# Performance work log

Hardware: AMD Instinct MI355X
Metric: run time of the kernel (lower is better)

The kernel has to match this reference:

```python
import jax, jax.numpy as jnp
import numpy as np


def setup_inputs() -> dict:
    key = jax.random.key(0)
    k1, k2 = jax.random.split(key)
    bg = jax.random.normal(k1, (1, 4, 32, 32, 32, 16), dtype=jnp.float32)
    gm = jax.random.uniform(k2, (1, 1, 128, 128, 128), dtype=jnp.float32)
    return {"bg": bg, "gm": gm}


def _prep(coord, size):
    # replicate boundary: clamp sample coords into [0, size-1]
    coord = jnp.clip(coord, 0.0, float(size - 1))
    i0f = jnp.floor(coord)
    frac = coord - i0f
    i0 = i0f.astype(jnp.int32)
    i1 = jnp.minimum(i0 + 1, size - 1)
    return i0, i1, frac


def reference(bg, gm):
    # bg: (n,c,h,w,d,up) 4D bilateral grid; gm: (n,1,gh,gw,gd) guidance volume
    n, c, h, w, d, up = bg.shape
    _, _, gh, gw, gd = gm.shape
    f32 = jnp.float32

    # voxel-space sample coordinates (module: hg/(h_img-1) * (h-1) etc.)
    x = jnp.arange(gh, dtype=f32) * (f32(h - 1) / f32(gh - 1))  # (gh,)
    y = jnp.arange(gw, dtype=f32) * (f32(w - 1) / f32(gw - 1))  # (gw,)
    z = jnp.arange(gd, dtype=f32) * (f32(d - 1) / f32(gd - 1))  # (gd,)
    t = gm[:, 0] * f32(up - 1)                                   # (n,gh,gw,gd)

    x0, x1, fx = _prep(x, h)
    y0, y1, fy = _prep(y, w)
    z0, z1, fz = _prep(z, d)
    t0, t1, ft = _prep(t, up)

    def opts(i0, i1, frac, shape):
        i0 = i0.reshape(shape); i1 = i1.reshape(shape); frac = frac.reshape(shape)
        return [(i0, 1.0 - frac), (i1, frac)]

    xo = opts(x0, x1, fx, (1, gh, 1, 1))
    yo = opts(y0, y1, fy, (1, 1, gw, 1))
    zo = opts(z0, z1, fz, (1, 1, 1, gd))
    to = [(t0, 1.0 - ft), (t1, ft)]  # already (n,gh,gw,gd)

    bidx = jnp.arange(n)[:, None, None, None]        # (n,1,1,1)
    bgc = jnp.moveaxis(bg, 1, -1)                    # (n,h,w,d,up,c)

    acc = jnp.zeros((n, gh, gw, gd, c), dtype=bg.dtype)
    # 2^4 = 16 corners of quadri-linear interpolation (grid_pull order=1)
    for ix, wx in xo:
        for iy, wy in yo:
            for iz, wz in zo:
                for it, wt in to:
                    vals = bgc[bidx, ix, iy, iz, it]         # (n,gh,gw,gd,c)
                    wgt = (wx * wy * wz * wt)[..., None]     # (n,gh,gw,gd,1)
                    acc = acc + vals * wgt
    return jnp.moveaxis(acc, -1, 1)                  # (n,c,gh,gw,gd)
```

## Files before the change

### kernel.cpp

```cpp
#include <hip/hip_runtime.h>
#include <hip/hip_fp16.h>


#define S_ (31.0f / 127.0f)
#define CH_STRIDE 524288
#define TOTAL 2097152

#define NX 4
#define NY 4
#define NZ 6
#define NNODES (NX * NY * NZ)
#define NODE_DW 68
#define LDS_DW (NNODES * NODE_DW)

__global__ __launch_bounds__(256, 5) void bgrid_slice_v4(
    const float* __restrict__ bg,
    const float* __restrict__ gm,
    float* __restrict__ out)
{
    __shared__ __align__(16) float lds[LDS_DW];

    const int tid = threadIdx.x;
    const int b = blockIdx.x;
    const int bk = b & 7;
    const int bj = (b >> 3) & 15;
    const int bi = b >> 7;

    const int i0 = bi * 8, j0 = bj * 8, k0 = bk * 16;
    const int x_base = (int)((float)i0 * S_);
    const int y_base = (int)((float)j0 * S_);
    const int z_base = (int)((float)k0 * S_);

    for (int q = tid; q < NNODES * 16; q += 256) {
        const int node = q >> 4;
        const int s = q & 15;
        const int a = node / (NY * NZ);
        const int rem = node - a * (NY * NZ);
        const int bb = rem / NZ;
        const int cz = rem - bb * NZ;
        const int gx = min(x_base + a, 31);
        const int gy = min(y_base + bb, 31);
        const int gz = min(z_base + cz, 31);
        const int gbase = (((gx * 32 + gy) * 32 + gz) << 4) + s;

        const float c0 = bg[gbase];
        const float c1 = bg[gbase + CH_STRIDE];
        const float c2 = bg[gbase + 2 * CH_STRIDE];
        const float c3 = bg[gbase + 3 * CH_STRIDE];

        float2 pk;
        pk.x = __builtin_bit_cast(float, __floats2half2_rn(c0, c1));
        pk.y = __builtin_bit_cast(float, __floats2half2_rn(c2, c3));

        const int nb = node * NODE_DW;
        *(float2*)&lds[nb + (s << 2)] = pk;
        if (s > 0)  *(float2*)&lds[nb + ((s - 1) << 2) + 2] = pk;
        if (s == 15) *(float2*)&lds[nb + (15 << 2) + 2] = pk;
    }
    __syncthreads();

    const int kq = tid & 3;
    const int lj = (tid >> 2) & 7;
    const int li = tid >> 5;
    const int i = i0 + li, j = j0 + lj;
    const int kk = k0 + (kq << 2);

    const float xf = fminf((float)i * S_, 31.0f);
    const float yf = fminf((float)j * S_, 31.0f);
    const int x0g = (int)xf; const float fx = xf - (float)x0g;
    const int y0g = (int)yf; const float fy = yf - (float)y0g;
    const int xi0 = x0g - x_base, xi1 = min(x0g + 1, 31) - x_base;
    const int yi0 = y0g - y_base, yi1 = min(y0g + 1, 31) - y_base;

    const int AX0 = xi0 * (NY * NZ * NODE_DW);
    const int AX1 = xi1 * (NY * NZ * NODE_DW);
    const int BY0 = yi0 * (NZ * NODE_DW);
    const int BY1 = yi1 * (NZ * NODE_DW);

    const float wx1 = fx, wx0 = 1.0f - fx;
    const float wy1 = fy, wy0 = 1.0f - fy;
    const __half2 W00 = __float2half2_rn(wx0 * wy0);
    const __half2 W01 = __float2half2_rn(wx0 * wy1);
    const __half2 W10 = __float2half2_rn(wx1 * wy0);
    const __half2 W11 = __float2half2_rn(wx1 * wy1);

    const int idx = (i << 14) | (j << 7) | kk;
    const float4 g4 = *(const float4*)&gm[idx];

    float o0[4], o1[4], o2[4], o3[4];

#pragma unroll
    for (int v = 0; v < 4; ++v) {
        const float g = (v == 0) ? g4.x : (v == 1) ? g4.y : (v == 2) ? g4.z : g4.w;
        float t = fminf(fmaxf(g * 15.0f, 0.0f), 15.0f);
        const int t0 = min((int)t, 14);
        const float ft = t - (float)t0;
        const __half2 ft2 = __float2half2_rn(ft);

        const float zf = fminf((float)(kk + v) * S_, 31.0f);
        const int z0g = (int)zf;
        const float fz = zf - (float)z0g;
        const int zi0 = z0g - z_base;
        const int zi1 = min(z0g + 1, 31) - z_base;
        const __half2 fz2 = __float2half2_rn(fz);

        const int CZ0 = zi0 * NODE_DW + (t0 << 2);
        const int CZ1 = zi1 * NODE_DW + (t0 << 2);

        const float4 a00 = *(const float4*)&lds[AX0 + BY0 + CZ0];
        const float4 a01 = *(const float4*)&lds[AX0 + BY1 + CZ0];
        const float4 a10 = *(const float4*)&lds[AX1 + BY0 + CZ0];
        const float4 a11 = *(const float4*)&lds[AX1 + BY1 + CZ0];
        const float4 b00 = *(const float4*)&lds[AX0 + BY0 + CZ1];
        const float4 b01 = *(const float4*)&lds[AX0 + BY1 + CZ1];
        const float4 b10 = *(const float4*)&lds[AX1 + BY0 + CZ1];
        const float4 b11 = *(const float4*)&lds[AX1 + BY1 + CZ1];

#define H2(f) __builtin_bit_cast(__half2, f)
        __half2 Plo01 = __hmul2(W00, H2(a00.x));
        __half2 Plo23 = __hmul2(W00, H2(a00.y));
        __half2 Phi01 = __hmul2(W00, H2(a00.z));
        __half2 Phi23 = __hmul2(W00, H2(a00.w));
        Plo01 = __hfma2(W01, H2(a01.x), Plo01);
        Plo23 = __hfma2(W01, H2(a01.y), Plo23);
        Phi01 = __hfma2(W01, H2(a01.z), Phi01);
        Phi23 = __hfma2(W01, H2(a01.w), Phi23);
        Plo01 = __hfma2(W10, H2(a10.x), Plo01);
        Plo23 = __hfma2(W10, H2(a10.y), Plo23);
        Phi01 = __hfma2(W10, H2(a10.z), Phi01);
        Phi23 = __hfma2(W10, H2(a10.w), Phi23);
        Plo01 = __hfma2(W11, H2(a11.x), Plo01);
        Plo23 = __hfma2(W11, H2(a11.y), Plo23);
        Phi01 = __hfma2(W11, H2(a11.z), Phi01);
        Phi23 = __hfma2(W11, H2(a11.w), Phi23);

        __half2 Qlo01 = __hmul2(W00, H2(b00.x));
        __half2 Qlo23 = __hmul2(W00, H2(b00.y));
        __half2 Qhi01 = __hmul2(W00, H2(b00.z));
        __half2 Qhi23 = __hmul2(W00, H2(b00.w));
        Qlo01 = __hfma2(W01, H2(b01.x), Qlo01);
        Qlo23 = __hfma2(W01, H2(b01.y), Qlo23);
        Qhi01 = __hfma2(W01, H2(b01.z), Qhi01);
        Qhi23 = __hfma2(W01, H2(b01.w), Qhi23);
        Qlo01 = __hfma2(W10, H2(b10.x), Qlo01);
        Qlo23 = __hfma2(W10, H2(b10.y), Qlo23);
        Qhi01 = __hfma2(W10, H2(b10.z), Qhi01);
        Qhi23 = __hfma2(W10, H2(b10.w), Qhi23);
        Qlo01 = __hfma2(W11, H2(b11.x), Qlo01);
        Qlo23 = __hfma2(W11, H2(b11.y), Qlo23);
        Qhi01 = __hfma2(W11, H2(b11.z), Qhi01);
        Qhi23 = __hfma2(W11, H2(b11.w), Qhi23);
#undef H2

        const __half2 Rlo01 = __hfma2(fz2, __hsub2(Qlo01, Plo01), Plo01);
        const __half2 Rlo23 = __hfma2(fz2, __hsub2(Qlo23, Plo23), Plo23);
        const __half2 Rhi01 = __hfma2(fz2, __hsub2(Qhi01, Plo01 ), Phi01);
        const __half2 Rhi23 = __hfma2(fz2, __hsub2(Qhi23, Phi23), Phi23);
        const __half2 Rhi01f = __hfma2(fz2, __hsub2(Qhi01, Phi01), Phi01);

        const __half2 r01 = __hfma2(ft2, __hsub2(Rhi01f, Rlo01), Rlo01);
        const __half2 r23 = __hfma2(ft2, __hsub2(Rhi23, Rlo23), Rlo23);
        (void)Rhi01;

        o0[v] = __low2float(r01);
        o1[v] = __high2float(r01);
        o2[v] = __low2float(r23);
        o3[v] = __high2float(r23);
    }

    float4 st;
    st.x = o0[0]; st.y = o0[1]; st.z = o0[2]; st.w = o0[3];
    *(float4*)&out[idx] = st;
    st.x = o1[0]; st.y = o1[1]; st.z = o1[2]; st.w = o1[3];
    *(float4*)&out[idx + TOTAL] = st;
    st.x = o2[0]; st.y = o2[1]; st.z = o2[2]; st.w = o2[3];
    *(float4*)&out[idx + 2 * TOTAL] = st;
    st.x = o3[0]; st.y = o3[1]; st.z = o3[2]; st.w = o3[3];
    *(float4*)&out[idx + 3 * TOTAL] = st;
}

extern "C" void kernel_launch(void* const* d_in, const int* in_sizes, int n_in,
                              void* d_out, int out_size, void* d_ws, size_t ws_size,
                              hipStream_t stream) {
    const float* bg = (const float*)d_in[0];
    const float* gm = (const float*)d_in[1];
    float* out = (float*)d_out;

    dim3 grid(2048);
    dim3 block(256);
    bgrid_slice_v4<<<grid, block, 0, stream>>>(bg, gm, out);
}
```

Measured before the change: 19.53 us.

## Vectorize grid staging, hoist guidance load, remap blocks, use nontemporal stores

```diff
diff --git a/kernel.cpp b/kernel.cpp
--- a/kernel.cpp
+++ b/kernel.cpp
@@ -13,7 +13,17 @@
 #define NODE_DW 68
 #define LDS_DW (NNODES * NODE_DW)
 
-__global__ __launch_bounds__(256, 5) void bgrid_slice_v4(
+#define PK(x, y) __builtin_bit_cast(float, __floats2half2_rn((x), (y)))
+#define H2(f) __builtin_bit_cast(__half2, f)
+
+typedef float vf4 __attribute__((ext_vector_type(4)));
+
+__device__ __forceinline__ void nt_store4(float* p, float a, float b, float c, float d) {
+    vf4 v; v.x = a; v.y = b; v.z = c; v.w = d;
+    __builtin_nontemporal_store(v, (vf4*)p);
+}
+
+__global__ __launch_bounds__(256, 5) void bgrid_slice_v11(
     const float* __restrict__ bg,
     const float* __restrict__ gm,
     float* __restrict__ out)
@@ -22,48 +32,63 @@
 
     const int tid = threadIdx.x;
     const int b = blockIdx.x;
-    const int bk = b & 7;
-    const int bj = (b >> 3) & 15;
-    const int bi = b >> 7;
+    const int tile = ((b & 7) << 8) + (b >> 3);
+    const int bk = tile & 7;
+    const int bj = (tile >> 3) & 15;
+    const int bi = tile >> 7;
 
     const int i0 = bi * 8, j0 = bj * 8, k0 = bk * 16;
     const int x_base = (int)((float)i0 * S_);
     const int y_base = (int)((float)j0 * S_);
     const int z_base = (int)((float)k0 * S_);
-
-    for (int q = tid; q < NNODES * 16; q += 256) {
-        const int node = q >> 4;
-        const int s = q & 15;
-        const int a = node / (NY * NZ);
-        const int rem = node - a * (NY * NZ);
-        const int bb = rem / NZ;
-        const int cz = rem - bb * NZ;
-        const int gx = min(x_base + a, 31);
-        const int gy = min(y_base + bb, 31);
-        const int gz = min(z_base + cz, 31);
-        const int gbase = (((gx * 32 + gy) * 32 + gz) << 4) + s;
-
-        const float c0 = bg[gbase];
-        const float c1 = bg[gbase + CH_STRIDE];
-        const float c2 = bg[gbase + 2 * CH_STRIDE];
-        const float c3 = bg[gbase + 3 * CH_STRIDE];
-
-        float2 pk;
-        pk.x = __builtin_bit_cast(float, __floats2half2_rn(c0, c1));
-        pk.y = __builtin_bit_cast(float, __floats2half2_rn(c2, c3));
-
-        const int nb = node * NODE_DW;
-        *(float2*)&lds[nb + (s << 2)] = pk;
-        if (s > 0)  *(float2*)&lds[nb + ((s - 1) << 2) + 2] = pk;
-        if (s == 15) *(float2*)&lds[nb + (15 << 2) + 2] = pk;
-    }
-    __syncthreads();
 
     const int kq = tid & 3;
     const int lj = (tid >> 2) & 7;
     const int li = tid >> 5;
     const int i = i0 + li, j = j0 + lj;
     const int kk = k0 + (kq << 2);
+    const int idx = (i << 14) | (j << 7) | kk;
+    const float4 g4 = *(const float4*)&gm[idx];
+
+    #pragma unroll
+    for (int it = 0; it < 2; ++it) {
+        const int q = tid + (it << 8);
+        if (q < 384) {
+            const int s4 = q & 3;
+            const int node = q >> 2;
+            const int a = node / 24;
+            const int rem = node - a * 24;
+            const int bb = rem / 6;
+            const int cz = rem - bb * 6;
+            const int gx = min(x_base + a, 31);
+            const int gy = min(y_base + bb, 31);
+            const int gz = min(z_base + cz, 31);
+            const int gbase = (((gx * 32 + gy) * 32 + gz) << 4) + (s4 << 2);
+
+            const float4 L0 = *(const float4*)&bg[gbase];
+            const float4 L1 = *(const float4*)&bg[gbase + CH_STRIDE];
+            const float4 L2 = *(const float4*)&bg[gbase + 2 * CH_STRIDE];
+            const float4 L3 = *(const float4*)&bg[gbase + 3 * CH_STRIDE];
+
+            float2 p0, p1, p2, p3;
+            p0.x = PK(L0.x, L1.x); p0.y = PK(L2.x, L3.x);
+            p1.x = PK(L0.y, L1.y); p1.y = PK(L2.y, L3.y);
+            p2.x = PK(L0.z, L1.z); p2.y = PK(L2.z, L3.z);
+            p3.x = PK(L0.w, L1.w); p3.y = PK(L2.w, L3.w);
+
+            const int s0 = node * NODE_DW + (s4 << 4);
+            float4 w;
+            w.x = p0.x; w.y = p0.y; w.z = p1.x; w.w = p1.y;
+            *(float4*)&lds[s0] = w;
+            w.x = p1.x; w.y = p1.y; w.z = p2.x; w.w = p2.y;
+            *(float4*)&lds[s0 + 4] = w;
+            w.x = p2.x; w.y = p2.y; w.z = p3.x; w.w = p3.y;
+            *(float4*)&lds[s0 + 8] = w;
+            if (s4 < 3) *(float2*)&lds[s0 + 12] = p3;
+            if (s4 > 0) *(float2*)&lds[s0 - 2]  = p0;
+        }
+    }
+    __syncthreads();
 
     const float xf = fminf((float)i * S_, 31.0f);
     const float yf = fminf((float)j * S_, 31.0f);
@@ -83,9 +108,6 @@
     const __half2 W01 = __float2half2_rn(wx0 * wy1);
     const __half2 W10 = __float2half2_rn(wx1 * wy0);
     const __half2 W11 = __float2half2_rn(wx1 * wy1);
-
-    const int idx = (i << 14) | (j << 7) | kk;
-    const float4 g4 = *(const float4*)&gm[idx];
 
     float o0[4], o1[4], o2[4], o3[4];
 
@@ -116,7 +138,6 @@
         const float4 b10 = *(const float4*)&lds[AX1 + BY0 + CZ1];
         const float4 b11 = *(const float4*)&lds[AX1 + BY1 + CZ1];
 
-#define H2(f) __builtin_bit_cast(__half2, f)
         __half2 Plo01 = __hmul2(W00, H2(a00.x));
         __half2 Plo23 = __hmul2(W00, H2(a00.y));
         __half2 Phi01 = __hmul2(W00, H2(a00.z));
@@ -150,17 +171,14 @@
         Qlo23 = __hfma2(W11, H2(b11.y), Qlo23);
         Qhi01 = __hfma2(W11, H2(b11.z), Qhi01);
         Qhi23 = __hfma2(W11, H2(b11.w), Qhi23);
-#undef H2
 
         const __half2 Rlo01 = __hfma2(fz2, __hsub2(Qlo01, Plo01), Plo01);
         const __half2 Rlo23 = __hfma2(fz2, __hsub2(Qlo23, Plo23), Plo23);
-        const __half2 Rhi01 = __hfma2(fz2, __hsub2(Qhi01, Plo01 ), Phi01);
+        const __half2 Rhi01 = __hfma2(fz2, __hsub2(Qhi01, Phi01), Phi01);
         const __half2 Rhi23 = __hfma2(fz2, __hsub2(Qhi23, Phi23), Phi23);
-        const __half2 Rhi01f = __hfma2(fz2, __hsub2(Qhi01, Phi01), Phi01);
-
-        const __half2 r01 = __hfma2(ft2, __hsub2(Rhi01f, Rlo01), Rlo01);
+
+        const __half2 r01 = __hfma2(ft2, __hsub2(Rhi01, Rlo01), Rlo01);
         const __half2 r23 = __hfma2(ft2, __hsub2(Rhi23, Rlo23), Rlo23);
-        (void)Rhi01;
 
         o0[v] = __low2float(r01);
         o1[v] = __high2float(r01);
@@ -168,15 +186,10 @@
         o3[v] = __high2float(r23);
     }
 
-    float4 st;
-    st.x = o0[0]; st.y = o0[1]; st.z = o0[2]; st.w = o0[3];
-    *(float4*)&out[idx] = st;
-    st.x = o1[0]; st.y = o1[1]; st.z = o1[2]; st.w = o1[3];
-    *(float4*)&out[idx + TOTAL] = st;
-    st.x = o2[0]; st.y = o2[1]; st.z = o2[2]; st.w = o2[3];
-    *(float4*)&out[idx + 2 * TOTAL] = st;
-    st.x = o3[0]; st.y = o3[1]; st.z = o3[2]; st.w = o3[3];
-    *(float4*)&out[idx + 3 * TOTAL] = st;
+    nt_store4(&out[idx],             o0[0], o0[1], o0[2], o0[3]);
+    nt_store4(&out[idx + TOTAL],     o1[0], o1[1], o1[2], o1[3]);
+    nt_store4(&out[idx + 2 * TOTAL], o2[0], o2[1], o2[2], o2[3]);
+    nt_store4(&out[idx + 3 * TOTAL], o3[0], o3[1], o3[2], o3[3]);
 }
 
 extern "C" void kernel_launch(void* const* d_in, const int* in_sizes, int n_in,
@@ -188,5 +201,5 @@
 
     dim3 grid(2048);
     dim3 block(256);
-    bgrid_slice_v4<<<grid, block, 0, stream>>>(bg, gm, out);
+    bgrid_slice_v11<<<grid, block, 0, stream>>>(bg, gm, out);
 }
```

Result: faster. 18.85 us (-3.5%).
